# Optimization experiments

Hardware: AMD Instinct MI355X
Metric: run time of the kernel (lower is better)

The kernel has to match this reference:

```python
import jax, jax.numpy as jnp
import numpy as np

B, D_IN, HID, DEPTH = 16384, 128, 16, 8
N_INNER = 2 ** DEPTH - 1   # 255
N_LEAF = 2 ** DEPTH        # 256


def setup_inputs() -> dict:
    key = jax.random.key(0)
    ks = jax.random.split(key, 4)
    x = jax.random.normal(ks[0], (B, D_IN), jnp.float32)
    # Batched per-inner-node tiny MLP parameters (PyTorch stores one Sequential per node;
    # we stack them along a leading node axis so the math is identical but vectorized).
    W1 = jax.random.normal(ks[1], (N_INNER, D_IN, HID), jnp.float32) / np.sqrt(D_IN).astype(np.float32)
    b1 = jnp.zeros((N_INNER, HID), jnp.float32)
    W2 = jax.random.normal(ks[2], (N_INNER, HID), jnp.float32) / np.sqrt(HID).astype(np.float32)
    b2 = jnp.zeros((N_INNER,), jnp.float32)
    leaf = jax.random.normal(ks[3], (N_LEAF, 1), jnp.float32) * 0.1
    return {"x": x, "W1": W1, "b1": b1, "W2": W2, "b2": b2, "leaf": leaf}


def reference(x, W1, b1, W2, b2, leaf):
    b = x.shape[0]
    depth = int(np.log2(leaf.shape[0]))
    # All inner-node gates in one batched GEMM: p[b, n] = sigmoid(W2_n . relu(W1_n^T x_b + b1_n) + b2_n)
    h1 = jax.nn.relu(jnp.einsum('bi,nih->bnh', x, W1) + b1[None])  # [B, N_inner, hid]
    p = jax.nn.sigmoid(jnp.einsum('bnh,nh->bn', h1, W2) + b2[None])  # [B, N_inner]

    # Level-by-level probability propagation (heap-ordered nodes):
    # children of node j are 2j+1 (left, mass*(1-p)) and 2j+2 (right, mass*p).
    r = jnp.ones((b, 1), x.dtype)
    levels = []
    for l in range(depth):
        levels.append(r)
        pl = p[:, 2 ** l - 1: 2 ** (l + 1) - 1]  # probs of nodes at level l, [B, 2^l]
        # interleave (left, right) so child ordering matches heap indexing
        r = jnp.stack([r * (1.0 - pl), r * pl], axis=-1).reshape(b, 2 ** (l + 1))
    node_reach = jnp.concatenate(levels, axis=1)  # [B, N_inner]
    path_probs = r                                 # [B, N_leaf]

    h = (path_probs @ leaf)[:, 0]                  # [B]
    return (h, path_probs, p, node_reach)
```

## Files before the change

kernel.cpp:

```cpp
#include <hip/hip_runtime.h>

#define BATCH 16384
#define DIN   128
#define HIDN  16
#define NNODE 255
#define NLEAF 256
#define TR    16

typedef _Float16 half8 __attribute__((ext_vector_type(8)));
typedef _Float16 half4 __attribute__((ext_vector_type(4)));
typedef float   float4v __attribute__((ext_vector_type(4)));

__global__ __launch_bounds__(256) void k_pack(const float* __restrict__ x, const float* __restrict__ w1,
                                              const float* __restrict__ w2,
                                              half8* __restrict__ xp, half8* __restrict__ w1p,
                                              _Float16* __restrict__ w2h) {
    __shared__ float w[DIN * 17];
    int t = threadIdx.x;
    if (blockIdx.x < 1024) {
        int gid  = blockIdx.x * 256 + t;
        int lane = gid & 63;
        int kc   = (gid >> 6) & 3;
        int bt   = gid >> 8;
        const float4* src = (const float4*)(x + (size_t)(bt * 16 + (lane & 15)) * DIN + kc * 32 + ((lane >> 4) * 8));
        float4 v0 = src[0], v1 = src[1];
        half8 v;
        v[0] = (_Float16)v0.x; v[1] = (_Float16)v0.y; v[2] = (_Float16)v0.z; v[3] = (_Float16)v0.w;
        v[4] = (_Float16)v1.x; v[5] = (_Float16)v1.y; v[6] = (_Float16)v1.z; v[7] = (_Float16)v1.w;
        xp[gid] = v;
    } else {
        int n = blockIdx.x - 1024;
        const float4* src = (const float4*)(w1 + (size_t)n * (DIN * HIDN)) + t * 2;
        float4 a0 = src[0], a1 = src[1];
        int base = t * 8;
#pragma unroll
        for (int e = 0; e < 4; ++e) {
            int idx0 = base + e, idx1 = base + 4 + e;
            w[(idx0 >> 4) * 17 + (idx0 & 15)] = (&a0.x)[e];
            w[(idx1 >> 4) * 17 + (idx1 & 15)] = (&a1.x)[e];
        }
        __syncthreads();
        int L  = t & 63;
        int kc = t >> 6;
        int m  = L & 15;
        int k0 = kc * 32 + (L >> 4) * 8;
        half8 v;
#pragma unroll
        for (int j = 0; j < 8; ++j) v[j] = (_Float16)w[(k0 + j) * 17 + m];
        w1p[(size_t)n * 256 + t] = v;
        if (t < HIDN) w2h[n * HIDN + t] = (_Float16)w2[n * HIDN + t];
    }
}

__global__ __launch_bounds__(256, 4) void k_mlp(const half8* __restrict__ xp, const half8* __restrict__ w1p,
                                                const float* __restrict__ b1, const _Float16* __restrict__ w2h,
                                                const float* __restrict__ b2, float* __restrict__ p_ws) {
    int wv   = threadIdx.x >> 6;
    int lane = threadIdx.x & 63;
    int q    = lane >> 4;
    int bt0  = blockIdx.x * 16 + wv * 4;
    int n0   = blockIdx.y * 15;

    half8 bq[4][4];
#pragma unroll
    for (int t = 0; t < 4; ++t)
#pragma unroll
        for (int kc = 0; kc < 4; ++kc)
            bq[t][kc] = xp[(size_t)((bt0 + t) * 4 + kc) * 64 + lane];
    asm volatile("" ::: "memory");

    for (int i = 0; i < 15; ++i) {
        int n = n0 + i;
        half8 a[4];
#pragma unroll
        for (int kc = 0; kc < 4; ++kc) a[kc] = w1p[(size_t)(n * 4 + kc) * 64 + lane];
        float4 b1f = ((const float4*)(b1 + n * HIDN))[q];
        half4  a2  = *(const half4*)(w2h + n * HIDN + q * 4);
        float  b2v = b2[n];
#pragma unroll
        for (int t = 0; t < 4; ++t) {
            float4v acc = {b1f.x, b1f.y, b1f.z, b1f.w};
#pragma unroll
            for (int kc = 0; kc < 4; ++kc)
                acc = __builtin_amdgcn_mfma_f32_16x16x32_f16(a[kc], bq[t][kc], acc, 0, 0, 0);
            half4 rb;
#pragma unroll
            for (int r = 0; r < 4; ++r) rb[r] = (_Float16)fmaxf(acc[r], 0.f);
            float4v acc2 = {b2v, b2v, b2v, b2v};
            acc2 = __builtin_amdgcn_mfma_f32_16x16x16f16(a2, rb, acc2, 0, 0, 0);
            if (lane < 16)
                p_ws[(size_t)n * BATCH + (bt0 + t) * 16 + lane] = acc2[0];
        }
    }
}

__global__ __launch_bounds__(256) void k_tree(const float* __restrict__ p_ws, const float* __restrict__ leaf,
                                              float* __restrict__ h_out, float* __restrict__ pp_out,
                                              float* __restrict__ p_out, float* __restrict__ nr_out) {
    __shared__ float sp[TR][NNODE + 2];
    int wv   = threadIdx.x >> 6;
    int lane = threadIdx.x & 63;
    int b0   = blockIdx.x * TR;
    int t    = threadIdx.x;

#pragma unroll
    for (int i = 0; i < 16; ++i) {
        int idx = i * 256 + t;
        if (idx < NNODE * TR) {
            int n = idx >> 4, bl = idx & 15;
            float lg = p_ws[(size_t)n * BATCH + b0 + bl];
            sp[bl][n] = __builtin_amdgcn_rcpf(1.f + __builtin_amdgcn_exp2f(-1.44269504088896f * lg));
        }
    }
    __syncthreads();

    for (int r = 0; r < TR; ++r)
        if (t < NNODE)
            p_out[(size_t)(b0 + r) * NNODE + t] = sp[r][t];

    for (int rr = 0; rr < 4; ++rr) {
        int i = wv * 4 + rr;
        int b = b0 + i;
        const float* P = &sp[i][0];
        float* nr = nr_out + (size_t)b * NNODE;

        float pref = 1.f;
#pragma unroll
        for (int l = 0; l < 6; ++l) {
            if ((lane & ((1 << (6 - l)) - 1)) == 0) nr[(1 << l) - 1 + (lane >> (6 - l))] = pref;
            float pv  = P[(1 << l) - 1 + (lane >> (6 - l))];
            int  bit  = (lane >> (5 - l)) & 1;
            pref *= bit ? pv : (1.f - pv);
        }
        nr[63 + lane] = pref;
        float p6 = P[63 + lane];
        float pl = pref * (1.f - p6);
        float pr = pref * p6;
        nr[127 + 2 * lane] = pl;
        nr[128 + 2 * lane] = pr;
        float p7a = P[127 + 2 * lane];
        float p7b = P[128 + 2 * lane];
        float4 pp;
        pp.x = pl * (1.f - p7a);
        pp.y = pl * p7a;
        pp.z = pr * (1.f - p7b);
        pp.w = pr * p7b;
        *(float4*)(pp_out + (size_t)b * NLEAF + 4 * lane) = pp;
        const float4 lf = *(const float4*)(leaf + 4 * lane);
        float hs = pp.x * lf.x + pp.y * lf.y + pp.z * lf.z + pp.w * lf.w;
#pragma unroll
        for (int off = 1; off < 64; off <<= 1) hs += __shfl_xor(hs, off, 64);
        if (lane == 0) h_out[b] = hs;
    }
}

extern "C" void kernel_launch(void* const* d_in, const int* in_sizes, int n_in,
                              void* d_out, int out_size, void* d_ws, size_t ws_size,
                              hipStream_t stream) {
    const float* x    = (const float*)d_in[0];
    const float* W1   = (const float*)d_in[1];
    const float* b1   = (const float*)d_in[2];
    const float* W2   = (const float*)d_in[3];
    const float* b2   = (const float*)d_in[4];
    const float* leaf = (const float*)d_in[5];

    float* out    = (float*)d_out;
    float* h_out  = out;
    float* pp_out = out + BATCH;
    float* p_out  = pp_out + (size_t)BATCH * NLEAF;
    float* nr_out = p_out + (size_t)BATCH * NNODE;

    half8*    xp   = (half8*)d_ws;
    half8*    w1p  = xp + (size_t)1024 * 4 * 64;
    _Float16* w2h  = (_Float16*)(w1p + (size_t)NNODE * 256);
    float*    p_ws = (float*)((char*)w2h + ((NNODE * HIDN * 2 + 255) & ~255));

    hipLaunchKernelGGL(k_pack, dim3(1024 + NNODE), dim3(256), 0, stream, x, W1, W2, xp, w1p, w2h);
    hipLaunchKernelGGL(k_mlp,  dim3(64, 17), dim3(256), 0, stream, xp, w1p, b1, w2h, b2, p_ws);
    hipLaunchKernelGGL(k_tree, dim3(BATCH / TR), dim3(256), 0, stream,
                       p_ws, leaf, h_out, pp_out, p_out, nr_out);
}
```

Measured before the change: 124.9 us.

## Prefetch next node weights in MLP kernel and split nodes across more blocks

The MLP kernel now software-pipelines the per-node weight, bias and W2 loads, fetching node i+1's operands while node i's MFMAs run, and fully unrolls the node loop. The grid's node dimension goes from 17 blocks of 15 nodes to 51 blocks of 5 nodes, tripling the block count for more parallelism and latency hiding. The trade-off is that each block reloads its x fragments for fewer nodes, so redundant x traffic rises, and register pressure grows from the double-buffered operands.

```diff
diff --git a/kernel.cpp b/kernel.cpp
--- a/kernel.cpp
+++ b/kernel.cpp
@@ -59,7 +59,7 @@
     int lane = threadIdx.x & 63;
     int q    = lane >> 4;
     int bt0  = blockIdx.x * 16 + wv * 4;
-    int n0   = blockIdx.y * 15;
+    int n0   = blockIdx.y * 5;
 
     half8 bq[4][4];
 #pragma unroll
@@ -69,27 +69,43 @@
             bq[t][kc] = xp[(size_t)((bt0 + t) * 4 + kc) * 64 + lane];
     asm volatile("" ::: "memory");
 
-    for (int i = 0; i < 15; ++i) {
+    half8 a_cur[4];
+#pragma unroll
+    for (int kc = 0; kc < 4; ++kc) a_cur[kc] = w1p[(size_t)(n0 * 4 + kc) * 64 + lane];
+    float4 b1_cur = ((const float4*)(b1 + n0 * HIDN))[q];
+    half4  a2_cur = *(const half4*)(w2h + n0 * HIDN + q * 4);
+    float  b2_cur = b2[n0];
+
+#pragma unroll
+    for (int i = 0; i < 5; ++i) {
         int n = n0 + i;
-        half8 a[4];
+        half8 a_nxt[4]; float4 b1_nxt; half4 a2_nxt; float b2_nxt;
+        if (i < 4) {
+            int m = n + 1;
 #pragma unroll
-        for (int kc = 0; kc < 4; ++kc) a[kc] = w1p[(size_t)(n * 4 + kc) * 64 + lane];
-        float4 b1f = ((const float4*)(b1 + n * HIDN))[q];
-        half4  a2  = *(const half4*)(w2h + n * HIDN + q * 4);
-        float  b2v = b2[n];
+            for (int kc = 0; kc < 4; ++kc) a_nxt[kc] = w1p[(size_t)(m * 4 + kc) * 64 + lane];
+            b1_nxt = ((const float4*)(b1 + m * HIDN))[q];
+            a2_nxt = *(const half4*)(w2h + m * HIDN + q * 4);
+            b2_nxt = b2[m];
+        }
 #pragma unroll
         for (int t = 0; t < 4; ++t) {
-            float4v acc = {b1f.x, b1f.y, b1f.z, b1f.w};
+            float4v acc = {b1_cur.x, b1_cur.y, b1_cur.z, b1_cur.w};
 #pragma unroll
             for (int kc = 0; kc < 4; ++kc)
-                acc = __builtin_amdgcn_mfma_f32_16x16x32_f16(a[kc], bq[t][kc], acc, 0, 0, 0);
+                acc = __builtin_amdgcn_mfma_f32_16x16x32_f16(a_cur[kc], bq[t][kc], acc, 0, 0, 0);
             half4 rb;
 #pragma unroll
             for (int r = 0; r < 4; ++r) rb[r] = (_Float16)fmaxf(acc[r], 0.f);
-            float4v acc2 = {b2v, b2v, b2v, b2v};
-            acc2 = __builtin_amdgcn_mfma_f32_16x16x16f16(a2, rb, acc2, 0, 0, 0);
+            float4v acc2 = {b2_cur, b2_cur, b2_cur, b2_cur};
+            acc2 = __builtin_amdgcn_mfma_f32_16x16x16f16(a2_cur, rb, acc2, 0, 0, 0);
             if (lane < 16)
                 p_ws[(size_t)n * BATCH + (bt0 + t) * 16 + lane] = acc2[0];
+        }
+        if (i < 4) {
+#pragma unroll
+            for (int kc = 0; kc < 4; ++kc) a_cur[kc] = a_nxt[kc];
+            b1_cur = b1_nxt; a2_cur = a2_nxt; b2_cur = b2_nxt;
         }
     }
 }
@@ -176,7 +192,7 @@
     float*    p_ws = (float*)((char*)w2h + ((NNODE * HIDN * 2 + 255) & ~255));
 
     hipLaunchKernelGGL(k_pack, dim3(1024 + NNODE), dim3(256), 0, stream, x, W1, W2, xp, w1p, w2h);
-    hipLaunchKernelGGL(k_mlp,  dim3(64, 17), dim3(256), 0, stream, xp, w1p, b1, w2h, b2, p_ws);
+    hipLaunchKernelGGL(k_mlp,  dim3(64, 51), dim3(256), 0, stream, xp, w1p, b1, w2h, b2, p_ws);
     hipLaunchKernelGGL(k_tree, dim3(BATCH / TR), dim3(256), 0, stream,
                        p_ws, leaf, h_out, pp_out, p_out, nr_out);
 }
```

New measurement: 130.5 us. +4.4%, slower.
